# Optimization experiments

Measured on AMD Instinct MI355X. Metric: run time of the kernel, lower is better.

Reference implementation:

```python
import jax, jax.numpy as jnp
import numpy as np

E, F, H = 8, 5632, 2048
T = 8192


def setup_inputs() -> dict:
    key = jax.random.key(0)
    k1, k2, k3, k4 = jax.random.split(key, 4)
    s_w = 1.0 / np.sqrt(H)
    return {
        "expert_idx": 3,
        "hidden_states": jax.random.normal(k1, (T, H), dtype=jnp.float32),
        "fc1_1": jax.random.normal(k2, (E, F, H), dtype=jnp.float32) * s_w,
        "fc1_2": jax.random.normal(k3, (E, F, H), dtype=jnp.float32) * s_w,
        "fc2": jax.random.normal(k4, (E, H, F), dtype=jnp.float32) * (1.0 / np.sqrt(F)),
    }


def reference(expert_idx, hidden_states, fc1_1, fc1_2, fc2):
    # Select this expert's weights: [F,H], [F,H], [H,F]
    w1 = fc1_1[expert_idx]
    w2 = fc1_2[expert_idx]
    w3 = fc2[expert_idx]
    # SwiGLU FFN: silu(x @ w1^T) * (x @ w2^T) @ w3^T
    gate = jnp.einsum("th,fh->tf", hidden_states, w1)
    up = jnp.einsum("th,fh->tf", hidden_states, w2)
    fc1_out = jax.nn.silu(gate) * up  # [T, F]
    out = jnp.einsum("tf,hf->th", fc1_out, w3)  # [T, H]
    return out
```

## Files before the change

### kernel.cpp

```cpp
#include <hip/hip_runtime.h>
#include <hip/hip_bf16.h>

#define T_DIM 8192
#define H_DIM 2048
#define F_DIM 5632

typedef __attribute__((ext_vector_type(4))) float f32x4;
typedef __attribute__((ext_vector_type(8))) short bf16x8;

static __device__ __forceinline__ void gload16(const void* g, void* l) {
    __builtin_amdgcn_global_load_lds(
        (const __attribute__((address_space(1))) void*)g,
        (__attribute__((address_space(3))) void*)l,
        16, 0, 0);
}

static __device__ __forceinline__ unsigned short f2bf(float f) {
    unsigned int u = __float_as_uint(f);
    u += 0x7fffu + ((u >> 16) & 1u);
    return (unsigned short)(u >> 16);
}

static __device__ __forceinline__ float bf2f(unsigned short u) {
    return __uint_as_float(((unsigned int)u) << 16);
}

__global__ __launch_bounds__(256)
void cvt_f32_bf16(const float* __restrict__ base, const int* __restrict__ eidx,
                  long per_expert, unsigned short* __restrict__ dst, long n)
{
    const float* src = base;
    if (eidx) src += (long)(*eidx) * per_expert;
    const long stride = (long)gridDim.x * blockDim.x;
    for (long i = (long)blockIdx.x * blockDim.x + threadIdx.x; i * 4 < n; i += stride) {
        const float4 v = *(const float4*)(src + i * 4);
        ushort4 o;
        o.x = f2bf(v.x); o.y = f2bf(v.y); o.z = f2bf(v.z); o.w = f2bf(v.w);
        *(ushort4*)(dst + i * 4) = o;
    }
}

static __device__ __forceinline__ void stage_half(const unsigned short* __restrict__ g,
                                                  long grow0, long ldk, long kb,
                                                  unsigned short* l, int t, int i0)
{
    const int r  = t >> 3;
    const int cc = ((t & 7) ^ (r & 7)) << 3;
    #pragma unroll
    for (int i = i0; i < i0 + 2; ++i)
        gload16(g + (grow0 + i * 64 + r) * ldk + kb + cc,
                l + i * 4096 + t * 8);
}

static __device__ __forceinline__ bf16x8 ldsfrag(const unsigned short* base,
                                                 int row, int kk, int q)
{
    return *(const bf16x8*)(base + row * 64 + (((kk * 4 + q) ^ (row & 7)) << 3));
}

#define PHASE_BODY(p, STAGE_STMT)                                              \
    {                                                                          \
        bf16x8 af[2][2];                                                       \
        _Pragma("unroll")                                                      \
        for (int l_ = 0; l_ < 2; ++l_)                                         \
            _Pragma("unroll")                                                  \
            for (int kk = 0; kk < 2; ++kk)                                     \
                af[l_][kk] = ldsfrag(la, wm * 128 + (p) * 32 + l_ * 16 + lr, kk, q); \
        STAGE_STMT;                                                            \
        __builtin_amdgcn_s_barrier();                                          \
        __builtin_amdgcn_s_setprio(1);                                         \
        _Pragma("unroll")                                                      \
        for (int l_ = 0; l_ < 2; ++l_)                                         \
            _Pragma("unroll")                                                  \
            for (int ni = 0; ni < 4; ++ni)                                     \
                _Pragma("unroll")                                              \
                for (int kk = 0; kk < 2; ++kk)                                 \
                    acc[(p) * 2 + l_][ni] = __builtin_amdgcn_mfma_f32_16x16x32_bf16( \
                        af[l_][kk], bf[ni][kk], acc[(p) * 2 + l_][ni], 0, 0, 0);     \
        __builtin_amdgcn_s_setprio(0);                                         \
        __builtin_amdgcn_s_barrier();                                          \
    }

template<int MODE, int KDIM, int NBN>
__global__ __launch_bounds__(512, 2)
void gemm256(const unsigned short* __restrict__ A,
             const unsigned short* __restrict__ B,
             void* outp, const unsigned short* gate)
{
    constexpr int  NK   = KDIM / 64;
    constexpr long NTOT = (long)NBN * 256;

    __shared__ __align__(16) unsigned short sAll[4 * 16384];

    const int tid  = threadIdx.x;
    const int lane = tid & 63;
    const int wid  = tid >> 6;
    const int wm   = wid >> 2;
    const int wn   = wid & 3;
    const int q    = lane >> 4;
    const int lr   = lane & 15;

    const int nwg = gridDim.x;
    const int bid = blockIdx.x;
    const int cpx = nwg >> 3;
    const int swz = (bid & 7) * cpx + (bid >> 3);
    const int bm  = swz / NBN;
    const int bn  = swz % NBN;

    const long arow0 = (long)bm * 256;
    const long brow0 = (long)bn * 256;

    f32x4 acc[8][4] = {};

    stage_half(A, arow0, KDIM, 0,  sAll,          tid, 0);
    stage_half(A, arow0, KDIM, 0,  sAll,          tid, 2);
    stage_half(B, brow0, KDIM, 0,  sAll + 16384,  tid, 0);
    stage_half(B, brow0, KDIM, 0,  sAll + 16384,  tid, 2);
    stage_half(B, brow0, KDIM, 64, sAll + 49152,  tid, 0);
    stage_half(B, brow0, KDIM, 64, sAll + 49152,  tid, 2);

    for (int j = 0; j < NK; ++j) {
        unsigned short* la = sAll + (j & 1) * 32768;
        unsigned short* lb = la + 16384;

        if (j + 1 < NK) {
            unsigned short* na = sAll + ((j + 1) & 1) * 32768;
            stage_half(A, arow0, KDIM, (long)(j + 1) * 64, na, tid, 0);
            stage_half(A, arow0, KDIM, (long)(j + 1) * 64, na, tid, 2);
            asm volatile("s_waitcnt vmcnt(8)" ::: "memory");
        } else {
            asm volatile("s_waitcnt vmcnt(0)" ::: "memory");
        }
        __builtin_amdgcn_s_barrier();

        bf16x8 bf[4][2];
        #pragma unroll
        for (int ni = 0; ni < 4; ++ni)
            #pragma unroll
            for (int kk = 0; kk < 2; ++kk)
                bf[ni][kk] = ldsfrag(lb, wn * 64 + ni * 16 + lr, kk, q);

        PHASE_BODY(0, {})
        PHASE_BODY(1, { if (j + 2 < NK) stage_half(B, brow0, KDIM, (long)(j + 2) * 64, lb, tid, 0); })
        PHASE_BODY(2, { if (j + 2 < NK) stage_half(B, brow0, KDIM, (long)(j + 2) * 64, lb, tid, 2); })
        PHASE_BODY(3, {})
    }

    const long orow = (long)bm * 256 + wm * 128;
    const long ocol = (long)bn * 256 + wn * 64;
    #pragma unroll
    for (int mi = 0; mi < 8; ++mi)
        #pragma unroll
        for (int ni = 0; ni < 4; ++ni)
            #pragma unroll
            for (int r = 0; r < 4; ++r) {
                const long idx = (orow + mi * 16 + q * 4 + r) * NTOT + (ocol + ni * 16 + lr);
                if constexpr (MODE == 0) {
                    ((float*)outp)[idx] = acc[mi][ni][r];
                } else if constexpr (MODE == 1) {
                    ((unsigned short*)outp)[idx] = f2bf(acc[mi][ni][r]);
                } else {
                    const float g = bf2f(gate[idx]);
                    const float h = __fdividef(g, 1.0f + __expf(-g)) * acc[mi][ni][r];
                    ((unsigned short*)outp)[idx] = f2bf(h);
                }
            }
}

extern "C" void kernel_launch(void* const* d_in, const int* in_sizes, int n_in,
                              void* d_out, int out_size, void* d_ws, size_t ws_size,
                              hipStream_t stream)
{
    const int*   eidx = (const int*)d_in[0];
    const float* x    = (const float*)d_in[1];
    const float* w1   = (const float*)d_in[2];
    const float* w2   = (const float*)d_in[3];
    const float* w3   = (const float*)d_in[4];
    float* out = (float*)d_out;

    unsigned short* Xb  = (unsigned short*)d_ws;
    unsigned short* W1b = Xb  + (long)T_DIM * H_DIM;
    unsigned short* W2b = W1b + (long)F_DIM * H_DIM;
    unsigned short* W3b = W2b + (long)F_DIM * H_DIM;
    unsigned short* Hb  = W3b + (long)H_DIM * F_DIM;

    cvt_f32_bf16<<<2048, 256, 0, stream>>>(x,  nullptr, 0, Xb, (long)T_DIM * H_DIM);
    cvt_f32_bf16<<<2048, 256, 0, stream>>>(w1, eidx, (long)F_DIM * H_DIM, W1b, (long)F_DIM * H_DIM);
    cvt_f32_bf16<<<2048, 256, 0, stream>>>(w2, eidx, (long)F_DIM * H_DIM, W2b, (long)F_DIM * H_DIM);
    cvt_f32_bf16<<<2048, 256, 0, stream>>>(w3, eidx, (long)H_DIM * F_DIM, W3b, (long)H_DIM * F_DIM);

    gemm256<1, H_DIM, F_DIM / 256><<<(T_DIM / 256) * (F_DIM / 256), 512, 0, stream>>>(
        Xb, W1b, Hb, nullptr);
    gemm256<2, H_DIM, F_DIM / 256><<<(T_DIM / 256) * (F_DIM / 256), 512, 0, stream>>>(
        Xb, W2b, Hb, Hb);
    gemm256<0, F_DIM, H_DIM / 256><<<(T_DIM / 256) * (H_DIM / 256), 512, 0, stream>>>(
        Hb, W3b, out, nullptr);
}
```

Before: 637.1 us.

## Store gate GEMM output in tile-blocked layout and prefetch it before last K step

Merges the three weight conversion kernels into a single launch. The gate GEMM now writes its bf16 output in a per-tile blocked layout with contiguous 8-byte stores per thread, replacing scattered 2-byte stores. The up GEMM peels its last K iteration and loads the gate values into registers before that final MFMA block, so the load latency overlaps with compute. This needs extra workspace for a separate gate buffer, falls back to the old path when the workspace is too small, and costs 32 extra ushort4 registers per thread.

```diff
diff --git a/kernel.cpp b/kernel.cpp
--- a/kernel.cpp
+++ b/kernel.cpp
@@ -26,17 +26,37 @@
 }
 
 __global__ __launch_bounds__(256)
-void cvt_f32_bf16(const float* __restrict__ base, const int* __restrict__ eidx,
-                  long per_expert, unsigned short* __restrict__ dst, long n)
-{
-    const float* src = base;
-    if (eidx) src += (long)(*eidx) * per_expert;
+void cvt_x(const float* __restrict__ src, unsigned short* __restrict__ dst, long n)
+{
     const long stride = (long)gridDim.x * blockDim.x;
     for (long i = (long)blockIdx.x * blockDim.x + threadIdx.x; i * 4 < n; i += stride) {
         const float4 v = *(const float4*)(src + i * 4);
         ushort4 o;
         o.x = f2bf(v.x); o.y = f2bf(v.y); o.z = f2bf(v.z); o.w = f2bf(v.w);
         *(ushort4*)(dst + i * 4) = o;
+    }
+}
+
+__global__ __launch_bounds__(256)
+void cvt_w(const float* __restrict__ w1, const float* __restrict__ w2,
+           const float* __restrict__ w3, const int* __restrict__ eidx,
+           unsigned short* __restrict__ W1b, unsigned short* __restrict__ W2b,
+           unsigned short* __restrict__ W3b)
+{
+    const long seg = (long)F_DIM * H_DIM;
+    const long e   = (long)(*eidx);
+    const long nchunks = 3 * seg / 4;
+    const long stride = (long)gridDim.x * blockDim.x;
+    for (long i = (long)blockIdx.x * blockDim.x + threadIdx.x; i < nchunks; i += stride) {
+        const long t = i * 4;
+        const int  s = (int)(t / seg);
+        const long o = t - (long)s * seg;
+        const float* src = (s == 0 ? w1 : s == 1 ? w2 : w3) + e * seg + o;
+        unsigned short* dst = (s == 0 ? W1b : s == 1 ? W2b : W3b) + o;
+        const float4 v = *(const float4*)src;
+        ushort4 ov;
+        ov.x = f2bf(v.x); ov.y = f2bf(v.y); ov.z = f2bf(v.z); ov.w = f2bf(v.w);
+        *(ushort4*)dst = ov;
     }
 }
 
@@ -85,7 +105,7 @@
 __global__ __launch_bounds__(512, 2)
 void gemm256(const unsigned short* __restrict__ A,
              const unsigned short* __restrict__ B,
-             void* outp, const unsigned short* gate)
+             void* outp, unsigned short* gate)
 {
     constexpr int  NK   = KDIM / 64;
     constexpr long NTOT = (long)NBN * 256;
@@ -109,6 +129,7 @@
 
     const long arow0 = (long)bm * 256;
     const long brow0 = (long)bn * 256;
+    const long tileBase = ((long)bm * NBN + bn) * 65536L;
 
     f32x4 acc[8][4] = {};
 
@@ -119,18 +140,13 @@
     stage_half(B, brow0, KDIM, 64, sAll + 49152,  tid, 0);
     stage_half(B, brow0, KDIM, 64, sAll + 49152,  tid, 2);
 
-    for (int j = 0; j < NK; ++j) {
+    for (int j = 0; j < NK - 1; ++j) {
         unsigned short* la = sAll + (j & 1) * 32768;
         unsigned short* lb = la + 16384;
-
-        if (j + 1 < NK) {
-            unsigned short* na = sAll + ((j + 1) & 1) * 32768;
-            stage_half(A, arow0, KDIM, (long)(j + 1) * 64, na, tid, 0);
-            stage_half(A, arow0, KDIM, (long)(j + 1) * 64, na, tid, 2);
-            asm volatile("s_waitcnt vmcnt(8)" ::: "memory");
-        } else {
-            asm volatile("s_waitcnt vmcnt(0)" ::: "memory");
-        }
+        unsigned short* na = sAll + ((j + 1) & 1) * 32768;
+        stage_half(A, arow0, KDIM, (long)(j + 1) * 64, na, tid, 0);
+        stage_half(A, arow0, KDIM, (long)(j + 1) * 64, na, tid, 2);
+        asm volatile("s_waitcnt vmcnt(8)" ::: "memory");
         __builtin_amdgcn_s_barrier();
 
         bf16x8 bf[4][2];
@@ -146,25 +162,71 @@
         PHASE_BODY(3, {})
     }
 
-    const long orow = (long)bm * 256 + wm * 128;
-    const long ocol = (long)bn * 256 + wn * 64;
-    #pragma unroll
-    for (int mi = 0; mi < 8; ++mi)
+    ushort4 pre[32];
+    {
+        const int j = NK - 1;
+        unsigned short* la = sAll + (j & 1) * 32768;
+        unsigned short* lb = la + 16384;
+        asm volatile("s_waitcnt vmcnt(0)" ::: "memory");
+        __builtin_amdgcn_s_barrier();
+
+        if constexpr (MODE == 4) {
+            #pragma unroll
+            for (int mi = 0; mi < 8; ++mi)
+                #pragma unroll
+                for (int ni = 0; ni < 4; ++ni)
+                    pre[mi * 4 + ni] = *(const ushort4*)(
+                        gate + tileBase + (long)(mi * 4 + ni) * 2048 + (long)tid * 4);
+        }
+
+        bf16x8 bf[4][2];
         #pragma unroll
         for (int ni = 0; ni < 4; ++ni)
             #pragma unroll
-            for (int r = 0; r < 4; ++r) {
-                const long idx = (orow + mi * 16 + q * 4 + r) * NTOT + (ocol + ni * 16 + lr);
-                if constexpr (MODE == 0) {
-                    ((float*)outp)[idx] = acc[mi][ni][r];
-                } else if constexpr (MODE == 1) {
-                    ((unsigned short*)outp)[idx] = f2bf(acc[mi][ni][r]);
-                } else {
-                    const float g = bf2f(gate[idx]);
-                    const float h = __fdividef(g, 1.0f + __expf(-g)) * acc[mi][ni][r];
-                    ((unsigned short*)outp)[idx] = f2bf(h);
+            for (int kk = 0; kk < 2; ++kk)
+                bf[ni][kk] = ldsfrag(lb, wn * 64 + ni * 16 + lr, kk, q);
+
+        PHASE_BODY(0, {})
+        PHASE_BODY(1, {})
+        PHASE_BODY(2, {})
+        PHASE_BODY(3, {})
+    }
+
+    if constexpr (MODE == 3) {
+        #pragma unroll
+        for (int mi = 0; mi < 8; ++mi)
+            #pragma unroll
+            for (int ni = 0; ni < 4; ++ni) {
+                ushort4 o;
+                o.x = f2bf(acc[mi][ni][0]); o.y = f2bf(acc[mi][ni][1]);
+                o.z = f2bf(acc[mi][ni][2]); o.w = f2bf(acc[mi][ni][3]);
+                *(ushort4*)(gate + tileBase + (long)(mi * 4 + ni) * 2048 + (long)tid * 4) = o;
+            }
+    } else {
+        const long orow = (long)bm * 256 + wm * 128;
+        const long ocol = (long)bn * 256 + wn * 64;
+        #pragma unroll
+        for (int mi = 0; mi < 8; ++mi)
+            #pragma unroll
+            for (int ni = 0; ni < 4; ++ni)
+                #pragma unroll
+                for (int r = 0; r < 4; ++r) {
+                    const long idx = (orow + mi * 16 + q * 4 + r) * NTOT + (ocol + ni * 16 + lr);
+                    if constexpr (MODE == 0) {
+                        ((float*)outp)[idx] = acc[mi][ni][r];
+                    } else if constexpr (MODE == 1) {
+                        ((unsigned short*)outp)[idx] = f2bf(acc[mi][ni][r]);
+                    } else if constexpr (MODE == 2) {
+                        const float g = bf2f(gate[idx]);
+                        const float h = __fdividef(g, 1.0f + __expf(-g)) * acc[mi][ni][r];
+                        ((unsigned short*)outp)[idx] = f2bf(h);
+                    } else {
+                        const float g = bf2f((&pre[mi * 4 + ni].x)[r]);
+                        const float h = __fdividef(g, 1.0f + __expf(-g)) * acc[mi][ni][r];
+                        ((unsigned short*)outp)[idx] = f2bf(h);
+                    }
                 }
-            }
+    }
 }
 
 extern "C" void kernel_launch(void* const* d_in, const int* in_sizes, int n_in,
@@ -178,21 +240,33 @@
     const float* w3   = (const float*)d_in[4];
     float* out = (float*)d_out;
 
+    const size_t SZ_X = (size_t)T_DIM * H_DIM;
+    const size_t SZ_W = (size_t)F_DIM * H_DIM;
+    const size_t SZ_H = (size_t)T_DIM * F_DIM;
+
     unsigned short* Xb  = (unsigned short*)d_ws;
-    unsigned short* W1b = Xb  + (long)T_DIM * H_DIM;
-    unsigned short* W2b = W1b + (long)F_DIM * H_DIM;
-    unsigned short* W3b = W2b + (long)F_DIM * H_DIM;
-    unsigned short* Hb  = W3b + (long)H_DIM * F_DIM;
-
-    cvt_f32_bf16<<<2048, 256, 0, stream>>>(x,  nullptr, 0, Xb, (long)T_DIM * H_DIM);
-    cvt_f32_bf16<<<2048, 256, 0, stream>>>(w1, eidx, (long)F_DIM * H_DIM, W1b, (long)F_DIM * H_DIM);
-    cvt_f32_bf16<<<2048, 256, 0, stream>>>(w2, eidx, (long)F_DIM * H_DIM, W2b, (long)F_DIM * H_DIM);
-    cvt_f32_bf16<<<2048, 256, 0, stream>>>(w3, eidx, (long)H_DIM * F_DIM, W3b, (long)H_DIM * F_DIM);
-
-    gemm256<1, H_DIM, F_DIM / 256><<<(T_DIM / 256) * (F_DIM / 256), 512, 0, stream>>>(
-        Xb, W1b, Hb, nullptr);
-    gemm256<2, H_DIM, F_DIM / 256><<<(T_DIM / 256) * (F_DIM / 256), 512, 0, stream>>>(
-        Xb, W2b, Hb, Hb);
-    gemm256<0, F_DIM, H_DIM / 256><<<(T_DIM / 256) * (H_DIM / 256), 512, 0, stream>>>(
-        Hb, W3b, out, nullptr);
-}
+    unsigned short* W1b = Xb  + SZ_X;
+    unsigned short* W2b = W1b + SZ_W;
+    unsigned short* W3b = W2b + SZ_W;
+    unsigned short* Hb  = W3b + SZ_W;
+    unsigned short* Gb  = Hb  + SZ_H;
+
+    const size_t need_blocked = (SZ_X + 3 * SZ_W + 2 * SZ_H) * 2;
+
+    cvt_x<<<2048, 256, 0, stream>>>(x, Xb, (long)SZ_X);
+    cvt_w<<<2048, 256, 0, stream>>>(w1, w2, w3, eidx, W1b, W2b, W3b);
+
+    constexpr int NBN1 = F_DIM / 256;
+    constexpr int NBN2 = H_DIM / 256;
+    const int grid1 = (T_DIM / 256) * NBN1;
+    const int grid2 = (T_DIM / 256) * NBN2;
+
+    if (ws_size >= need_blocked) {
+        gemm256<3, H_DIM, NBN1><<<grid1, 512, 0, stream>>>(Xb, W1b, nullptr, Gb);
+        gemm256<4, H_DIM, NBN1><<<grid1, 512, 0, stream>>>(Xb, W2b, Hb, Gb);
+    } else {
+        gemm256<1, H_DIM, NBN1><<<grid1, 512, 0, stream>>>(Xb, W1b, Hb, nullptr);
+        gemm256<2, H_DIM, NBN1><<<grid1, 512, 0, stream>>>(Xb, W2b, Hb, Hb);
+    }
+    gemm256<0, F_DIM, NBN2><<<grid2, 512, 0, stream>>>(Hb, W3b, out, nullptr);
+}
```

Result: faster. 599.4 us (-5.9%).
